# Kernel optimization log

Hardware: AMD Instinct MI355X
Metric: run time of the kernel (lower is better)

The kernel has to match this reference:

```python
import jax, jax.numpy as jnp
import numpy as np


def setup_inputs() -> dict:
    key = jax.random.key(0)
    ks = jax.random.split(key, 7)
    B, C, N, D = 32, 256, 4096, 256
    s = 0.05
    return {
        "x": jax.random.normal(ks[0], (B, C, N), dtype=jnp.float32),
        "Wq": jax.random.normal(ks[1], (D, C), dtype=jnp.float32) * s,
        "bq": jax.random.normal(ks[2], (D,), dtype=jnp.float32) * s,
        "Wk": jax.random.normal(ks[3], (D, C), dtype=jnp.float32) * s,
        "bk": jax.random.normal(ks[4], (D,), dtype=jnp.float32) * s,
        "Wv": jax.random.normal(ks[5], (D, C), dtype=jnp.float32) * s,
        "bv": jax.random.normal(ks[6], (D,), dtype=jnp.float32) * s,
    }


def reference(x, Wq, bq, Wk, bk, Wv, bv):
    # 1x1 Conv1d == per-timestep linear: [B,C,N] x [D,C] -> [B,D,N]
    Q = jnp.einsum("bcn,dc->bdn", x, Wq) + bq[None, :, None]
    K = jnp.einsum("bcn,dc->bdn", x, Wk) + bk[None, :, None]
    V = jnp.einsum("bcn,dc->bdn", x, Wv) + bv[None, :, None]
    N = x.shape[-1]
    scale = 1.0 / jnp.sqrt(jnp.asarray(N, dtype=x.dtype))
    # channel-attention: scores are [B, D, D] (Q @ K^T over the time axis)
    scores = jnp.einsum("bdn,ben->bde", Q, K) * scale
    weights = jax.nn.softmax(scores, axis=-1)
    out = jnp.einsum("bde,ben->bdn", weights, V)  # [B, D, N]
    return out
```

## Files before the change

### kernel.cpp

```cpp
#include <hip/hip_runtime.h>
#include <cstdint>
#include <cstddef>


typedef float f32x4 __attribute__((ext_vector_type(4)));
typedef __bf16 bf16x8 __attribute__((ext_vector_type(8)));
typedef unsigned short u16;
typedef u16 u16x8 __attribute__((ext_vector_type(8)));
typedef u16 u16x4 __attribute__((ext_vector_type(4)));

__device__ __forceinline__ u16 f2bf(float f) {
    unsigned u = __builtin_bit_cast(unsigned, f);
    u += 0x7FFFu + ((u >> 16) & 1u);
    return (u16)(u >> 16);
}

__device__ __forceinline__ f32x4 mfma16(bf16x8 a, bf16x8 b, f32x4 c) {
    return __builtin_amdgcn_mfma_f32_16x16x32_bf16(a, b, c, 0, 0, 0);
}

__global__ void k_wvt(const float* __restrict__ Wv, u16* __restrict__ WvT) {
    const int eb = blockIdx.x;
    const int c  = threadIdx.x;
    u16x8 pk;
#pragma unroll
    for (int j = 0; j < 8; ++j) pk[j] = f2bf(Wv[(eb * 8 + j) * 256 + c]);
    *(u16x8*)&WvT[c * 256 + eb * 8] = pk;
}

__global__ void k_wcvt(const float* __restrict__ Wq, const float* __restrict__ Wk,
                       u16* __restrict__ Wqb, u16* __restrict__ Wkb) {
    const int m = blockIdx.x >> 5, chunk = blockIdx.x & 31;
    const float* src = m == 0 ? Wq : Wk;
    u16* dst = m == 0 ? Wqb : Wkb;
    const int i = chunk * 2048 + threadIdx.x * 8;
    f32x4 w0 = *(const f32x4*)(src + i);
    f32x4 w1 = *(const f32x4*)(src + i + 4);
    u16x8 pk;
    pk[0] = f2bf(w0[0]); pk[1] = f2bf(w0[1]); pk[2] = f2bf(w0[2]); pk[3] = f2bf(w0[3]);
    pk[4] = f2bf(w1[0]); pk[5] = f2bf(w1[1]); pk[6] = f2bf(w1[2]); pk[7] = f2bf(w1[3]);
    *(u16x8*)&dst[i] = pk;
}

__global__ __launch_bounds__(512, 2) void k_gram_p(const float* __restrict__ x,
                                                   float* __restrict__ Gpart,
                                                   float* __restrict__ rsum) {
    __shared__ __align__(16) u16 lds[2][256 * 64];
    __shared__ float ldsr[256];
    const int b = blockIdx.x >> 3, split = blockIdx.x & 7;
    const int t = threadIdx.x;
    const int lane = t & 63, wid = t >> 6;
    const int g = lane >> 4, q = lane & 15;

    if (t < 256) ldsr[t] = 0.f;

    f32x4 zero4 = {0.f, 0.f, 0.f, 0.f};
    f32x4 acc[2][16];
#pragma unroll
    for (int i = 0; i < 2; ++i)
#pragma unroll
        for (int j = 0; j < 16; ++j) acc[i][j] = zero4;

    const int c_st = t >> 1, half = t & 1;
    const int swz_w = (c_st & 7) << 3;
    const float* xp = x + ((size_t)b * 256 + c_st) * 4096 + split * 512 + half * 32;

    float s = 0.f;
    f32x4 R[8];
#pragma unroll
    for (int j = 0; j < 8; ++j) R[j] = *(const f32x4*)(xp + j * 4);
#pragma unroll
    for (int kk = 0; kk < 4; ++kk) {
        f32x4 w0 = R[2 * kk], w1 = R[2 * kk + 1];
        s += w0[0] + w0[1] + w0[2] + w0[3] + w1[0] + w1[1] + w1[2] + w1[3];
        u16x8 pk;
        pk[0] = f2bf(w0[0]); pk[1] = f2bf(w0[1]); pk[2] = f2bf(w0[2]); pk[3] = f2bf(w0[3]);
        pk[4] = f2bf(w1[0]); pk[5] = f2bf(w1[1]); pk[6] = f2bf(w1[2]); pk[7] = f2bf(w1[3]);
        *(u16x8*)&lds[0][(c_st * 64 + half * 32 + kk * 8) ^ swz_w] = pk;
    }
    __syncthreads();

    for (int nc = 0; nc < 8; ++nc) {
        const int cur = nc & 1;
        if (nc < 7) {
#pragma unroll
            for (int j = 0; j < 8; ++j) R[j] = *(const f32x4*)(xp + (nc + 1) * 64 + j * 4);
        }
#pragma unroll
        for (int ks = 0; ks < 2; ++ks) {
            const int c0 = 32 * wid + q;
            const int c1 = c0 + 16;
            bf16x8 a0 = *(const bf16x8*)&lds[cur][(c0 * 64 + ks * 32 + g * 8) ^ ((c0 & 7) << 3)];
            bf16x8 a1 = *(const bf16x8*)&lds[cur][(c1 * 64 + ks * 32 + g * 8) ^ ((c1 & 7) << 3)];
#pragma unroll
            for (int et = 0; et < 16; ++et) {
                const int c2 = et * 16 + q;
                bf16x8 bb = *(const bf16x8*)&lds[cur][(c2 * 64 + ks * 32 + g * 8) ^ ((c2 & 7) << 3)];
                acc[0][et] = mfma16(a0, bb, acc[0][et]);
                acc[1][et] = mfma16(a1, bb, acc[1][et]);
            }
        }
        if (nc < 7) {
#pragma unroll
            for (int kk = 0; kk < 4; ++kk) {
                f32x4 w0 = R[2 * kk], w1 = R[2 * kk + 1];
                s += w0[0] + w0[1] + w0[2] + w0[3] + w1[0] + w1[1] + w1[2] + w1[3];
                u16x8 pk;
                pk[0] = f2bf(w0[0]); pk[1] = f2bf(w0[1]); pk[2] = f2bf(w0[2]); pk[3] = f2bf(w0[3]);
                pk[4] = f2bf(w1[0]); pk[5] = f2bf(w1[1]); pk[6] = f2bf(w1[2]); pk[7] = f2bf(w1[3]);
                *(u16x8*)&lds[cur ^ 1][(c_st * 64 + half * 32 + kk * 8) ^ swz_w] = pk;
            }
        }
        __syncthreads();
    }

    atomicAdd(&ldsr[c_st], s);

    float* gp = Gpart + (size_t)(split * 32 + b) * 65536;
#pragma unroll
    for (int dt = 0; dt < 2; ++dt)
#pragma unroll
        for (int et = 0; et < 16; ++et)
#pragma unroll
            for (int rr = 0; rr < 4; ++rr) {
                const int cc = 32 * wid + dt * 16 + 4 * g + rr;
                const int c2 = et * 16 + q;
                gp[cc * 256 + c2] = acc[dt][et][rr];
            }
    __syncthreads();
    if (t < 256) atomicAdd(&rsum[b * 256 + t], ldsr[t]);
}

__global__ void k_reduce(const float* __restrict__ Gpart, u16* __restrict__ Gb) {
    const size_t j = (size_t)blockIdx.x * 2048 + threadIdx.x * 8;
    f32x4 s0 = {0.f, 0.f, 0.f, 0.f}, s1 = {0.f, 0.f, 0.f, 0.f};
#pragma unroll
    for (int s = 0; s < 8; ++s) {
        s0 += *(const f32x4*)(Gpart + (size_t)s * 2097152 + j);
        s1 += *(const f32x4*)(Gpart + (size_t)s * 2097152 + j + 4);
    }
    u16x8 pk;
    pk[0] = f2bf(s0[0]); pk[1] = f2bf(s0[1]); pk[2] = f2bf(s0[2]); pk[3] = f2bf(s0[3]);
    pk[4] = f2bf(s1[0]); pk[5] = f2bf(s1[1]); pk[6] = f2bf(s1[2]); pk[7] = f2bf(s1[3]);
    *(u16x8*)&Gb[j] = pk;
}

__global__ __launch_bounds__(512, 2) void k_gram(const float* __restrict__ x,
                                                 float* __restrict__ G,
                                                 float* __restrict__ rsum) {
    __shared__ __align__(16) u16 lds[256 * 64];
    __shared__ float ldsr[256];
    const int b = blockIdx.x >> 3, split = blockIdx.x & 7;
    const int t = threadIdx.x;
    const int lane = t & 63, wid = t >> 6;
    const int g = lane >> 4, q = lane & 15;

    if (t < 256) ldsr[t] = 0.f;

    f32x4 zero4 = {0.f, 0.f, 0.f, 0.f};
    f32x4 acc[2][16];
#pragma unroll
    for (int i = 0; i < 2; ++i)
#pragma unroll
        for (int j = 0; j < 16; ++j) acc[i][j] = zero4;

    const int c_st = t >> 1, half = t & 1;
    const int swz_w = (c_st & 7) << 3;
    const float* xp = x + ((size_t)b * 256 + c_st) * 4096 + split * 512 + half * 32;

    for (int nc = 0; nc < 8; ++nc) {
        __syncthreads();
        float s = 0.f;
#pragma unroll
        for (int kk = 0; kk < 4; ++kk) {
            f32x4 w0 = *(const f32x4*)(xp + nc * 64 + kk * 8);
            f32x4 w1 = *(const f32x4*)(xp + nc * 64 + kk * 8 + 4);
            s += w0[0] + w0[1] + w0[2] + w0[3] + w1[0] + w1[1] + w1[2] + w1[3];
            u16x8 pk;
            pk[0] = f2bf(w0[0]); pk[1] = f2bf(w0[1]); pk[2] = f2bf(w0[2]); pk[3] = f2bf(w0[3]);
            pk[4] = f2bf(w1[0]); pk[5] = f2bf(w1[1]); pk[6] = f2bf(w1[2]); pk[7] = f2bf(w1[3]);
            *(u16x8*)&lds[(c_st * 64 + half * 32 + kk * 8) ^ swz_w] = pk;
        }
        atomicAdd(&ldsr[c_st], s);
        __syncthreads();
#pragma unroll
        for (int ks = 0; ks < 2; ++ks) {
            const int c0 = 32 * wid + q;
            const int c1 = c0 + 16;
            bf16x8 a0 = *(const bf16x8*)&lds[(c0 * 64 + ks * 32 + g * 8) ^ ((c0 & 7) << 3)];
            bf16x8 a1 = *(const bf16x8*)&lds[(c1 * 64 + ks * 32 + g * 8) ^ ((c1 & 7) << 3)];
#pragma unroll
            for (int et = 0; et < 16; ++et) {
                const int c2 = et * 16 + q;
                bf16x8 bb = *(const bf16x8*)&lds[(c2 * 64 + ks * 32 + g * 8) ^ ((c2 & 7) << 3)];
                acc[0][et] = mfma16(a0, bb, acc[0][et]);
                acc[1][et] = mfma16(a1, bb, acc[1][et]);
            }
        }
    }
#pragma unroll
    for (int dt = 0; dt < 2; ++dt)
#pragma unroll
        for (int et = 0; et < 16; ++et)
#pragma unroll
            for (int rr = 0; rr < 4; ++rr) {
                const int cc = 32 * wid + dt * 16 + 4 * g + rr;
                const int c2 = et * 16 + q;
                atomicAdd(&G[((size_t)b * 256 + cc) * 256 + c2], acc[dt][et][rr]);
            }
    __syncthreads();
    if (t < 256) atomicAdd(&rsum[b * 256 + t], ldsr[t]);
}

__global__ void k_gcvt(const float* __restrict__ G, u16* __restrict__ Gb) {
    const size_t i = (size_t)blockIdx.x * 2048 + threadIdx.x * 8;
    f32x4 w0 = *(const f32x4*)(G + i);
    f32x4 w1 = *(const f32x4*)(G + i + 4);
    u16x8 pk;
    pk[0] = f2bf(w0[0]); pk[1] = f2bf(w0[1]); pk[2] = f2bf(w0[2]); pk[3] = f2bf(w0[3]);
    pk[4] = f2bf(w1[0]); pk[5] = f2bf(w1[1]); pk[6] = f2bf(w1[2]); pk[7] = f2bf(w1[3]);
    *(u16x8*)&Gb[i] = pk;
}

__global__ __launch_bounds__(512, 4) void k_T(const u16* __restrict__ Gb,
                                              const u16* __restrict__ Wkb,
                                              u16* __restrict__ Tws) {
    const int b = blockIdx.x >> 3, ebase = (blockIdx.x & 7) * 32;
    const int t = threadIdx.x;
    const int lane = t & 63, wid = t >> 6;
    const int g = lane >> 4, q = lane & 15;

    f32x4 zero4 = {0.f, 0.f, 0.f, 0.f};
    f32x4 acc[2][2];
#pragma unroll
    for (int i = 0; i < 2; ++i)
#pragma unroll
        for (int j = 0; j < 2; ++j) acc[i][j] = zero4;

    const u16* gp = Gb + (size_t)b * 65536;
#pragma unroll
    for (int ks = 0; ks < 8; ++ks) {
        bf16x8 a0 = *(const bf16x8*)&gp[(32 * wid + q) * 256 + ks * 32 + g * 8];
        bf16x8 a1 = *(const bf16x8*)&gp[(32 * wid + 16 + q) * 256 + ks * 32 + g * 8];
        bf16x8 b0 = *(const bf16x8*)&Wkb[(ebase + q) * 256 + ks * 32 + g * 8];
        bf16x8 b1 = *(const bf16x8*)&Wkb[(ebase + 16 + q) * 256 + ks * 32 + g * 8];
        acc[0][0] = mfma16(a0, b0, acc[0][0]);
        acc[0][1] = mfma16(a0, b1, acc[0][1]);
        acc[1][0] = mfma16(a1, b0, acc[1][0]);
        acc[1][1] = mfma16(a1, b1, acc[1][1]);
    }
#pragma unroll
    for (int dt = 0; dt < 2; ++dt)
#pragma unroll
        for (int etl = 0; etl < 2; ++etl) {
            const int e = ebase + etl * 16 + q;
            const int cb = 32 * wid + dt * 16 + 4 * g;
            u16x4 pk;
            pk[0] = f2bf(acc[dt][etl][0]); pk[1] = f2bf(acc[dt][etl][1]);
            pk[2] = f2bf(acc[dt][etl][2]); pk[3] = f2bf(acc[dt][etl][3]);
            *(u16x4*)&Tws[((size_t)b * 256 + e) * 256 + cb] = pk;
        }
}

__global__ __launch_bounds__(256, 2) void k_SWM(
    const u16* __restrict__ Tws, const float* __restrict__ rsum,
    const float* __restrict__ Wq, const u16* __restrict__ Wqb,
    const float* __restrict__ Wk,
    const float* __restrict__ bqv, const float* __restrict__ bkv,
    const float* __restrict__ bvv,
    const u16* __restrict__ WvT, u16* __restrict__ Mws, float* __restrict__ cpv) {
    __shared__ __align__(16) u16 Wlds[64 * 256];
    __shared__ float r_[256], v_[256], bk_[256], bv_[256], u_[64], bq_[64];
    const int b = blockIdx.x >> 2, dbase = (blockIdx.x & 3) * 64;
    const int t = threadIdx.x;
    const int lane = t & 63, wid = t >> 6;
    const int g = lane >> 4, q = lane & 15;

    r_[t] = rsum[b * 256 + t];
    bk_[t] = bkv[t];
    bv_[t] = bvv[t];
    if (t < 64) bq_[t] = bqv[dbase + t];
    __syncthreads();

    {
        float s = 0.f; const float* wp = Wk + (size_t)t * 256;
#pragma unroll 4
        for (int c = 0; c < 256; c += 4) {
            f32x4 w = *(const f32x4*)(wp + c);
            f32x4 rr = *(const f32x4*)(&r_[c]);
            s += w[0] * rr[0] + w[1] * rr[1] + w[2] * rr[2] + w[3] * rr[3];
        }
        v_[t] = s;
    }
    if (t < 64) {
        float s = 0.f; const float* wp = Wq + (size_t)(dbase + t) * 256;
#pragma unroll 4
        for (int c = 0; c < 256; c += 4) {
            f32x4 w = *(const f32x4*)(wp + c);
            f32x4 rr = *(const f32x4*)(&r_[c]);
            s += w[0] * rr[0] + w[1] * rr[1] + w[2] * rr[2] + w[3] * rr[3];
        }
        u_[t] = s;
    }
    __syncthreads();

    f32x4 zero4 = {0.f, 0.f, 0.f, 0.f};
    f32x4 acc[16];
#pragma unroll
    for (int j = 0; j < 16; ++j) acc[j] = zero4;

    const u16* tp = Tws + (size_t)b * 65536;
    const int d_l = wid * 16 + q;
#pragma unroll 2
    for (int ks = 0; ks < 8; ++ks) {
        bf16x8 bb = *(const bf16x8*)&Wqb[(dbase + d_l) * 256 + ks * 32 + g * 8];
#pragma unroll
        for (int et = 0; et < 16; ++et) {
            bf16x8 aa = *(const bf16x8*)&tp[(et * 16 + q) * 256 + ks * 32 + g * 8];
            acc[et] = mfma16(aa, bb, acc[et]);
        }
    }

    {
        const float ud = u_[d_l], bqd = bq_[d_l];
        float m = -3.4e38f;
#pragma unroll
        for (int et = 0; et < 16; ++et)
#pragma unroll
            for (int rr = 0; rr < 4; ++rr) {
                const int e = et * 16 + 4 * g + rr;
                float s = (acc[et][rr] + ud * bk_[e] + bqd * v_[e] + 4096.f * bqd * bk_[e]) * 0.015625f;
                acc[et][rr] = s;
                m = fmaxf(m, s);
            }
        m = fmaxf(m, __shfl_xor(m, 16));
        m = fmaxf(m, __shfl_xor(m, 32));
        float lsum = 0.f;
#pragma unroll
        for (int et = 0; et < 16; ++et)
#pragma unroll
            for (int rr = 0; rr < 4; ++rr) {
                float p = __expf(acc[et][rr] - m);
                acc[et][rr] = p;
                lsum += p;
            }
        lsum += __shfl_xor(lsum, 16);
        lsum += __shfl_xor(lsum, 32);
        const float inv = 1.f / lsum;
        float cp = 0.f;
#pragma unroll
        for (int et = 0; et < 16; ++et)
#pragma unroll
            for (int rr = 0; rr < 4; ++rr) {
                const int e = et * 16 + 4 * g + rr;
                float w = acc[et][rr] * inv;
                acc[et][rr] = w;
                cp += w * bv_[e];
            }
        cp += __shfl_xor(cp, 16);
        cp += __shfl_xor(cp, 32);
        if (g == 0) cpv[b * 256 + dbase + d_l] = cp;
    }

#pragma unroll
    for (int et = 0; et < 16; ++et) {
        u16x4 pk;
        pk[0] = f2bf(acc[et][0]); pk[1] = f2bf(acc[et][1]);
        pk[2] = f2bf(acc[et][2]); pk[3] = f2bf(acc[et][3]);
        *(u16x4*)&Wlds[(d_l * 256 + et * 16 + 4 * g) ^ ((d_l & 7) << 3)] = pk;
    }
    __syncthreads();

    f32x4 acc2[4][4];
#pragma unroll
    for (int i = 0; i < 4; ++i)
#pragma unroll
        for (int j = 0; j < 4; ++j) acc2[i][j] = zero4;

#pragma unroll 2
    for (int ks = 0; ks < 8; ++ks) {
        bf16x8 afr[4], bfr[4];
#pragma unroll
        for (int ct = 0; ct < 4; ++ct)
            afr[ct] = *(const bf16x8*)&WvT[(64 * wid + ct * 16 + q) * 256 + ks * 32 + g * 8];
#pragma unroll
        for (int j = 0; j < 4; ++j) {
            const int dl = j * 16 + q;
            bfr[j] = *(const bf16x8*)&Wlds[(dl * 256 + ks * 32 + g * 8) ^ ((dl & 7) << 3)];
        }
#pragma unroll
        for (int ct = 0; ct < 4; ++ct)
#pragma unroll
            for (int j = 0; j < 4; ++j)
                acc2[ct][j] = mfma16(afr[ct], bfr[j], acc2[ct][j]);
    }
#pragma unroll
    for (int ct = 0; ct < 4; ++ct)
#pragma unroll
        for (int j = 0; j < 4; ++j) {
            const int d = dbase + j * 16 + q;
            const int cb = 64 * wid + ct * 16 + 4 * g;
            u16x4 pk;
            pk[0] = f2bf(acc2[ct][j][0]); pk[1] = f2bf(acc2[ct][j][1]);
            pk[2] = f2bf(acc2[ct][j][2]); pk[3] = f2bf(acc2[ct][j][3]);
            *(u16x4*)&Mws[((size_t)b * 256 + d) * 256 + cb] = pk;
        }
}

__global__ __launch_bounds__(512, 2) void k_out(const float* __restrict__ x,
                                                const u16* __restrict__ Mws,
                                                const float* __restrict__ cpv,
                                                float* __restrict__ out) {
    __shared__ __align__(16) u16 xt[256 * 64];
    __shared__ float cp_l[256];
    const int b = blockIdx.x >> 4, nt = blockIdx.x & 15;
    const int n0 = nt * 256;
    const int t = threadIdx.x;
    const int lane = t & 63, wid = t >> 6;
    const int g = lane >> 4, q = lane & 15;

    if (t < 256) cp_l[t] = cpv[b * 256 + t];

    f32x4 zero4 = {0.f, 0.f, 0.f, 0.f};
    f32x4 acc[2][16];
#pragma unroll
    for (int i = 0; i < 2; ++i)
#pragma unroll
        for (int j = 0; j < 16; ++j) acc[i][j] = zero4;

    const int c8 = t & 7;
    const int n4 = t >> 3;

    for (int cb = 0; cb < 256; cb += 64) {
        __syncthreads();
#pragma unroll
        for (int sub = 0; sub < 2; ++sub) {
            const int cc0 = cb + (c8 + 8 * sub) * 4;
            const float* xp = x + ((size_t)b * 256 + cc0) * 4096 + n0 + n4 * 4;
            f32x4 r0 = *(const f32x4*)(xp);
            f32x4 r1 = *(const f32x4*)(xp + 4096);
            f32x4 r2 = *(const f32x4*)(xp + 8192);
            f32x4 r3 = *(const f32x4*)(xp + 12288);
#pragma unroll
            for (int j = 0; j < 4; ++j) {
                const int n = n4 * 4 + j;
                u16x4 pk;
                pk[0] = f2bf(r0[j]); pk[1] = f2bf(r1[j]); pk[2] = f2bf(r2[j]); pk[3] = f2bf(r3[j]);
                *(u16x4*)&xt[(n * 64 + (c8 + 8 * sub) * 4) ^ ((n & 7) << 3)] = pk;
            }
        }
        __syncthreads();
#pragma unroll
        for (int ks = 0; ks < 2; ++ks) {
            bf16x8 a0 = *(const bf16x8*)&Mws[((size_t)b * 256 + (32 * wid + q)) * 256 + cb + ks * 32 + g * 8];
            bf16x8 a1 = *(const bf16x8*)&Mws[((size_t)b * 256 + (32 * wid + 16 + q)) * 256 + cb + ks * 32 + g * 8];
#pragma unroll
            for (int ntl = 0; ntl < 16; ++ntl) {
                const int nn = ntl * 16 + q;
                bf16x8 bb = *(const bf16x8*)&xt[(nn * 64 + ks * 32 + g * 8) ^ ((nn & 7) << 3)];
                acc[0][ntl] = mfma16(a0, bb, acc[0][ntl]);
                acc[1][ntl] = mfma16(a1, bb, acc[1][ntl]);
            }
        }
    }
#pragma unroll
    for (int dt = 0; dt < 2; ++dt)
#pragma unroll
        for (int ntl = 0; ntl < 16; ++ntl)
#pragma unroll
            for (int rr = 0; rr < 4; ++rr) {
                const int d = 32 * wid + dt * 16 + 4 * g + rr;
                const int n = n0 + ntl * 16 + q;
                out[((size_t)b * 256 + d) * 4096 + n] = acc[dt][ntl][rr] + cp_l[d];
            }
}

extern "C" void kernel_launch(void* const* d_in, const int* in_sizes, int n_in,
                              void* d_out, int out_size, void* d_ws, size_t ws_size,
                              hipStream_t stream) {
    const float* x  = (const float*)d_in[0];
    const float* Wq = (const float*)d_in[1];
    const float* bq = (const float*)d_in[2];
    const float* Wk = (const float*)d_in[3];
    const float* bk = (const float*)d_in[4];
    const float* Wv = (const float*)d_in[5];
    const float* bv = (const float*)d_in[6];
    float* out = (float*)d_out;
    char* ws = (char*)d_ws;

    const size_t NEED_FAST = 71761920;

    if (ws_size >= NEED_FAST) {
        float* Gpart = (float*)(ws);
        u16*   Tws   = (u16*)  (ws);
        u16*   Mws   = (u16*)  (ws + 4194304);
        u16*   Gb    = (u16*)  (ws + 67108864);
        float* rsum  = (float*)(ws + 71303168);
        float* cpv   = (float*)(ws + 71335936);
        u16*   WvT   = (u16*)  (ws + 71368704);
        u16*   Wqb   = (u16*)  (ws + 71499776);
        u16*   Wkb   = (u16*)  (ws + 71630848);

        hipMemsetAsync(ws + 71303168, 0, 32768, stream);

        hipLaunchKernelGGL(k_wvt,    dim3(32),   dim3(256), 0, stream, Wv, WvT);
        hipLaunchKernelGGL(k_wcvt,   dim3(64),   dim3(256), 0, stream, Wq, Wk, Wqb, Wkb);
        hipLaunchKernelGGL(k_gram_p, dim3(256),  dim3(512), 0, stream, x, Gpart, rsum);
        hipLaunchKernelGGL(k_reduce, dim3(1024), dim3(256), 0, stream, Gpart, Gb);
        hipLaunchKernelGGL(k_T,      dim3(256),  dim3(512), 0, stream, Gb, Wkb, Tws);
        hipLaunchKernelGGL(k_SWM,    dim3(128),  dim3(256), 0, stream,
                           Tws, rsum, Wq, Wqb, Wk, bq, bk, bv, WvT, Mws, cpv);
        hipLaunchKernelGGL(k_out,    dim3(512),  dim3(512), 0, stream, x, Mws, cpv, out);
    } else {
        float* G    = (float*)(ws);
        u16*   Tws  = (u16*)  (ws);
        u16*   Gb   = (u16*)  (ws + 8388608);
        u16*   Mws  = (u16*)  (ws + 8388608);
        float* rsum = (float*)(ws + 12582912);
        float* cpv  = (float*)(ws + 12615680);
        u16*   WvT  = (u16*)  (ws + 12648448);
        u16*   Wqb  = (u16*)  (ws + 12779520);
        u16*   Wkb  = (u16*)  (ws + 12910592);

        hipMemsetAsync(ws, 0, 8388608, stream);
        hipMemsetAsync(ws + 12582912, 0, 32768, stream);

        hipLaunchKernelGGL(k_wvt,  dim3(32),   dim3(256), 0, stream, Wv, WvT);
        hipLaunchKernelGGL(k_wcvt, dim3(64),   dim3(256), 0, stream, Wq, Wk, Wqb, Wkb);
        hipLaunchKernelGGL(k_gram, dim3(256),  dim3(512), 0, stream, x, G, rsum);
        hipLaunchKernelGGL(k_gcvt, dim3(1024), dim3(256), 0, stream, G, Gb);
        hipLaunchKernelGGL(k_T,    dim3(256),  dim3(512), 0, stream, Gb, Wkb, Tws);
        hipLaunchKernelGGL(k_SWM,  dim3(128),  dim3(256), 0, stream,
                           Tws, rsum, Wq, Wqb, Wk, bq, bk, bv, WvT, Mws, cpv);
        hipLaunchKernelGGL(k_out,  dim3(512),  dim3(512), 0, stream, x, Mws, cpv, out);
    }
}
```

Measured before the change: 200.0 us.

## Store bf16 Gram partials over 16 splits and restructure output GEMM tiling

The Gram partial kernel now splits the time axis 16 ways instead of 8 and writes its partial results as bf16 through swapped MFMA operands, so it can store packed vectors. The reduce kernel sums 16 bf16 partials in fp32. The output kernel now uses 256-thread blocks over 128-column tiles with a double-buffered LDS stage and register prefetch of x. Mws fragments are read directly from global memory, and each thread writes a vectorised f32x4 store. These changes aim to cut partial-buffer traffic, raise occupancy and overlap loads with MFMA, at the cost of extra bf16 rounding in the partial sums.

```diff
diff --git a/kernel.cpp b/kernel.cpp
--- a/kernel.cpp
+++ b/kernel.cpp
@@ -13,6 +13,10 @@
     unsigned u = __builtin_bit_cast(unsigned, f);
     u += 0x7FFFu + ((u >> 16) & 1u);
     return (u16)(u >> 16);
+}
+__device__ __forceinline__ float bf2f(u16 h) {
+    unsigned u = ((unsigned)h) << 16;
+    return __builtin_bit_cast(float, u);
 }
 
 __device__ __forceinline__ f32x4 mfma16(bf16x8 a, bf16x8 b, f32x4 c) {
@@ -42,12 +46,12 @@
     *(u16x8*)&dst[i] = pk;
 }
 
-__global__ __launch_bounds__(512, 2) void k_gram_p(const float* __restrict__ x,
-                                                   float* __restrict__ Gpart,
+__global__ __launch_bounds__(512, 4) void k_gram_p(const float* __restrict__ x,
+                                                   u16* __restrict__ Gpart,
                                                    float* __restrict__ rsum) {
     __shared__ __align__(16) u16 lds[2][256 * 64];
     __shared__ float ldsr[256];
-    const int b = blockIdx.x >> 3, split = blockIdx.x & 7;
+    const int b = blockIdx.x >> 4, split = blockIdx.x & 15;
     const int t = threadIdx.x;
     const int lane = t & 63, wid = t >> 6;
     const int g = lane >> 4, q = lane & 15;
@@ -63,7 +67,7 @@
 
     const int c_st = t >> 1, half = t & 1;
     const int swz_w = (c_st & 7) << 3;
-    const float* xp = x + ((size_t)b * 256 + c_st) * 4096 + split * 512 + half * 32;
+    const float* xp = x + ((size_t)b * 256 + c_st) * 4096 + split * 256 + half * 32;
 
     float s = 0.f;
     f32x4 R[8];
@@ -80,9 +84,9 @@
     }
     __syncthreads();
 
-    for (int nc = 0; nc < 8; ++nc) {
+    for (int nc = 0; nc < 4; ++nc) {
         const int cur = nc & 1;
-        if (nc < 7) {
+        if (nc < 3) {
 #pragma unroll
             for (int j = 0; j < 8; ++j) R[j] = *(const f32x4*)(xp + (nc + 1) * 64 + j * 4);
         }
@@ -96,11 +100,11 @@
             for (int et = 0; et < 16; ++et) {
                 const int c2 = et * 16 + q;
                 bf16x8 bb = *(const bf16x8*)&lds[cur][(c2 * 64 + ks * 32 + g * 8) ^ ((c2 & 7) << 3)];
-                acc[0][et] = mfma16(a0, bb, acc[0][et]);
-                acc[1][et] = mfma16(a1, bb, acc[1][et]);
-            }
-        }
-        if (nc < 7) {
+                acc[0][et] = mfma16(bb, a0, acc[0][et]);
+                acc[1][et] = mfma16(bb, a1, acc[1][et]);
+            }
+        }
+        if (nc < 3) {
 #pragma unroll
             for (int kk = 0; kk < 4; ++kk) {
                 f32x4 w0 = R[2 * kk], w1 = R[2 * kk + 1];
@@ -116,32 +120,35 @@
 
     atomicAdd(&ldsr[c_st], s);
 
-    float* gp = Gpart + (size_t)(split * 32 + b) * 65536;
+    u16* gp = Gpart + (size_t)(split * 32 + b) * 65536;
 #pragma unroll
     for (int dt = 0; dt < 2; ++dt)
 #pragma unroll
-        for (int et = 0; et < 16; ++et)
-#pragma unroll
-            for (int rr = 0; rr < 4; ++rr) {
-                const int cc = 32 * wid + dt * 16 + 4 * g + rr;
-                const int c2 = et * 16 + q;
-                gp[cc * 256 + c2] = acc[dt][et][rr];
-            }
+        for (int et = 0; et < 16; ++et) {
+            const int cc = 32 * wid + dt * 16 + q;
+            u16x4 pk;
+            pk[0] = f2bf(acc[dt][et][0]); pk[1] = f2bf(acc[dt][et][1]);
+            pk[2] = f2bf(acc[dt][et][2]); pk[3] = f2bf(acc[dt][et][3]);
+            *(u16x4*)&gp[cc * 256 + et * 16 + 4 * g] = pk;
+        }
     __syncthreads();
     if (t < 256) atomicAdd(&rsum[b * 256 + t], ldsr[t]);
 }
 
-__global__ void k_reduce(const float* __restrict__ Gpart, u16* __restrict__ Gb) {
-    const size_t j = (size_t)blockIdx.x * 2048 + threadIdx.x * 8;
-    f32x4 s0 = {0.f, 0.f, 0.f, 0.f}, s1 = {0.f, 0.f, 0.f, 0.f};
-#pragma unroll
-    for (int s = 0; s < 8; ++s) {
-        s0 += *(const f32x4*)(Gpart + (size_t)s * 2097152 + j);
-        s1 += *(const f32x4*)(Gpart + (size_t)s * 2097152 + j + 4);
+__global__ void k_reduce(const u16* __restrict__ Gpart, u16* __restrict__ Gb) {
+    const size_t j = ((size_t)blockIdx.x * 256 + threadIdx.x) * 8;
+    float s[8];
+#pragma unroll
+    for (int i = 0; i < 8; ++i) s[i] = 0.f;
+#pragma unroll
+    for (int sp = 0; sp < 16; ++sp) {
+        u16x8 v = *(const u16x8*)(Gpart + (size_t)sp * 2097152 + j);
+#pragma unroll
+        for (int i = 0; i < 8; ++i) s[i] += bf2f(v[i]);
     }
     u16x8 pk;
-    pk[0] = f2bf(s0[0]); pk[1] = f2bf(s0[1]); pk[2] = f2bf(s0[2]); pk[3] = f2bf(s0[3]);
-    pk[4] = f2bf(s1[0]); pk[5] = f2bf(s1[1]); pk[6] = f2bf(s1[2]); pk[7] = f2bf(s1[3]);
+#pragma unroll
+    for (int i = 0; i < 8; ++i) pk[i] = f2bf(s[i]);
     *(u16x8*)&Gb[j] = pk;
 }
 
@@ -407,19 +414,19 @@
         }
 }
 
-__global__ __launch_bounds__(512, 2) void k_out(const float* __restrict__ x,
+__global__ __launch_bounds__(256, 4) void k_out(const float* __restrict__ x,
                                                 const u16* __restrict__ Mws,
                                                 const float* __restrict__ cpv,
                                                 float* __restrict__ out) {
-    __shared__ __align__(16) u16 xt[256 * 64];
+    __shared__ __align__(16) u16 xt[2][128 * 64];
     __shared__ float cp_l[256];
-    const int b = blockIdx.x >> 4, nt = blockIdx.x & 15;
-    const int n0 = nt * 256;
+    const int b = blockIdx.x >> 5, nt = blockIdx.x & 31;
+    const int n0 = nt * 128;
     const int t = threadIdx.x;
     const int lane = t & 63, wid = t >> 6;
     const int g = lane >> 4, q = lane & 15;
 
-    if (t < 256) cp_l[t] = cpv[b * 256 + t];
+    cp_l[t] = cpv[b * 256 + t];
 
     f32x4 zero4 = {0.f, 0.f, 0.f, 0.f};
     f32x4 acc[2][16];
@@ -431,48 +438,78 @@
     const int c8 = t & 7;
     const int n4 = t >> 3;
 
-    for (int cb = 0; cb < 256; cb += 64) {
+    const float* xbase = x + (size_t)b * 256 * 4096 + n0 + n4 * 4;
+    const u16* mp = Mws + (size_t)b * 65536;
+
+    f32x4 R[2][4];
+#pragma unroll
+    for (int sub = 0; sub < 2; ++sub) {
+        const int cc0 = (c8 + 8 * sub) * 4;
+#pragma unroll
+        for (int j = 0; j < 4; ++j) R[sub][j] = *(const f32x4*)(xbase + (size_t)(cc0 + j) * 4096);
+    }
+#pragma unroll
+    for (int sub = 0; sub < 2; ++sub)
+#pragma unroll
+        for (int j = 0; j < 4; ++j) {
+            const int n = n4 * 4 + j;
+            u16x4 pk;
+            pk[0] = f2bf(R[sub][0][j]); pk[1] = f2bf(R[sub][1][j]);
+            pk[2] = f2bf(R[sub][2][j]); pk[3] = f2bf(R[sub][3][j]);
+            *(u16x4*)&xt[0][(n * 64 + (c8 + 8 * sub) * 4) ^ ((n & 7) << 3)] = pk;
+        }
+    __syncthreads();
+
+    for (int ci = 0; ci < 4; ++ci) {
+        const int cur = ci & 1;
+        if (ci < 3) {
+#pragma unroll
+            for (int sub = 0; sub < 2; ++sub) {
+                const int cc0 = (ci + 1) * 64 + (c8 + 8 * sub) * 4;
+#pragma unroll
+                for (int j = 0; j < 4; ++j) R[sub][j] = *(const f32x4*)(xbase + (size_t)(cc0 + j) * 4096);
+            }
+        }
+#pragma unroll
+        for (int ks = 0; ks < 2; ++ks) {
+            bf16x8 afr[2];
+#pragma unroll
+            for (int nt2 = 0; nt2 < 2; ++nt2) {
+                const int nl = 32 * wid + nt2 * 16 + q;
+                afr[nt2] = *(const bf16x8*)&xt[cur][(nl * 64 + ks * 32 + g * 8) ^ ((nl & 7) << 3)];
+            }
+#pragma unroll
+            for (int dtl = 0; dtl < 16; ++dtl) {
+                bf16x8 bfr = *(const bf16x8*)&mp[(dtl * 16 + q) * 256 + ci * 64 + ks * 32 + g * 8];
+                acc[0][dtl] = mfma16(afr[0], bfr, acc[0][dtl]);
+                acc[1][dtl] = mfma16(afr[1], bfr, acc[1][dtl]);
+            }
+        }
+        if (ci < 3) {
+#pragma unroll
+            for (int sub = 0; sub < 2; ++sub)
+#pragma unroll
+                for (int j = 0; j < 4; ++j) {
+                    const int n = n4 * 4 + j;
+                    u16x4 pk;
+                    pk[0] = f2bf(R[sub][0][j]); pk[1] = f2bf(R[sub][1][j]);
+                    pk[2] = f2bf(R[sub][2][j]); pk[3] = f2bf(R[sub][3][j]);
+                    *(u16x4*)&xt[cur ^ 1][(n * 64 + (c8 + 8 * sub) * 4) ^ ((n & 7) << 3)] = pk;
+                }
+        }
         __syncthreads();
-#pragma unroll
-        for (int sub = 0; sub < 2; ++sub) {
-            const int cc0 = cb + (c8 + 8 * sub) * 4;
-            const float* xp = x + ((size_t)b * 256 + cc0) * 4096 + n0 + n4 * 4;
-            f32x4 r0 = *(const f32x4*)(xp);
-            f32x4 r1 = *(const f32x4*)(xp + 4096);
-            f32x4 r2 = *(const f32x4*)(xp + 8192);
-            f32x4 r3 = *(const f32x4*)(xp + 12288);
-#pragma unroll
-            for (int j = 0; j < 4; ++j) {
-                const int n = n4 * 4 + j;
-                u16x4 pk;
-                pk[0] = f2bf(r0[j]); pk[1] = f2bf(r1[j]); pk[2] = f2bf(r2[j]); pk[3] = f2bf(r3[j]);
-                *(u16x4*)&xt[(n * 64 + (c8 + 8 * sub) * 4) ^ ((n & 7) << 3)] = pk;
-            }
-        }
-        __syncthreads();
-#pragma unroll
-        for (int ks = 0; ks < 2; ++ks) {
-            bf16x8 a0 = *(const bf16x8*)&Mws[((size_t)b * 256 + (32 * wid + q)) * 256 + cb + ks * 32 + g * 8];
-            bf16x8 a1 = *(const bf16x8*)&Mws[((size_t)b * 256 + (32 * wid + 16 + q)) * 256 + cb + ks * 32 + g * 8];
-#pragma unroll
-            for (int ntl = 0; ntl < 16; ++ntl) {
-                const int nn = ntl * 16 + q;
-                bf16x8 bb = *(const bf16x8*)&xt[(nn * 64 + ks * 32 + g * 8) ^ ((nn & 7) << 3)];
-                acc[0][ntl] = mfma16(a0, bb, acc[0][ntl]);
-                acc[1][ntl] = mfma16(a1, bb, acc[1][ntl]);
-            }
-        }
-    }
-#pragma unroll
-    for (int dt = 0; dt < 2; ++dt)
-#pragma unroll
-        for (int ntl = 0; ntl < 16; ++ntl)
-#pragma unroll
-            for (int rr = 0; rr < 4; ++rr) {
-                const int d = 32 * wid + dt * 16 + 4 * g + rr;
-                const int n = n0 + ntl * 16 + q;
-                out[((size_t)b * 256 + d) * 4096 + n] = acc[dt][ntl][rr] + cp_l[d];
-            }
+    }
+
+#pragma unroll
+    for (int nt2 = 0; nt2 < 2; ++nt2)
+#pragma unroll
+        for (int dtl = 0; dtl < 16; ++dtl) {
+            const int d = dtl * 16 + q;
+            const float cp = cp_l[d];
+            f32x4 v = acc[nt2][dtl];
+            v[0] += cp; v[1] += cp; v[2] += cp; v[3] += cp;
+            *(f32x4*)&out[((size_t)b * 256 + d) * 4096 + n0 + 32 * wid + nt2 * 16 + 4 * g] = v;
+        }
 }
 
 extern "C" void kernel_launch(void* const* d_in, const int* in_sizes, int n_in,
@@ -491,7 +528,7 @@
     const size_t NEED_FAST = 71761920;
 
     if (ws_size >= NEED_FAST) {
-        float* Gpart = (float*)(ws);
+        u16*   Gpart = (u16*)  (ws);
         u16*   Tws   = (u16*)  (ws);
         u16*   Mws   = (u16*)  (ws + 4194304);
         u16*   Gb    = (u16*)  (ws + 67108864);
@@ -505,12 +542,12 @@
 
         hipLaunchKernelGGL(k_wvt,    dim3(32),   dim3(256), 0, stream, Wv, WvT);
         hipLaunchKernelGGL(k_wcvt,   dim3(64),   dim3(256), 0, stream, Wq, Wk, Wqb, Wkb);
-        hipLaunchKernelGGL(k_gram_p, dim3(256),  dim3(512), 0, stream, x, Gpart, rsum);
+        hipLaunchKernelGGL(k_gram_p, dim3(512),  dim3(512), 0, stream, x, Gpart, rsum);
         hipLaunchKernelGGL(k_reduce, dim3(1024), dim3(256), 0, stream, Gpart, Gb);
         hipLaunchKernelGGL(k_T,      dim3(256),  dim3(512), 0, stream, Gb, Wkb, Tws);
         hipLaunchKernelGGL(k_SWM,    dim3(128),  dim3(256), 0, stream,
                            Tws, rsum, Wq, Wqb, Wk, bq, bk, bv, WvT, Mws, cpv);
-        hipLaunchKernelGGL(k_out,    dim3(512),  dim3(512), 0, stream, x, Mws, cpv, out);
+        hipLaunchKernelGGL(k_out,    dim3(1024), dim3(256), 0, stream, x, Mws, cpv, out);
     } else {
         float* G    = (float*)(ws);
         u16*   Tws  = (u16*)  (ws);
@@ -532,6 +569,6 @@
         hipLaunchKernelGGL(k_T,    dim3(256),  dim3(512), 0, stream, Gb, Wkb, Tws);
         hipLaunchKernelGGL(k_SWM,  dim3(128),  dim3(256), 0, stream,
                            Tws, rsum, Wq, Wqb, Wk, bq, bk, bv, WvT, Mws, cpv);
-        hipLaunchKernelGGL(k_out,  dim3(512),  dim3(512), 0, stream, x, Mws, cpv, out);
-    }
-}
+        hipLaunchKernelGGL(k_out,  dim3(1024), dim3(256), 0, stream, x, Mws, cpv, out);
+    }
+}
```

New measurement: 747.9 us. 3.74x slower.
